# Performance work log

Measured on AMD Instinct MI355X. Metric: run time of the kernel, lower is better.

Reference implementation:

```python
import jax, jax.numpy as jnp
import numpy as np

N_NODES = 10000
N_EDGES = 160000
NEG_SLOPE = 0.2


def _gat_layer(x, src, dst, W, a_src, a_dst, bias, concat):
    # x: [N, F_in]; W: [F_in, H*C]; a_src/a_dst: [H, C]; bias: [H*C] or [C]
    N = x.shape[0]
    H, C = a_src.shape
    h = (x @ W).reshape(N, H, C)                       # [N,H,C]
    al_s = jnp.einsum('nhc,hc->nh', h, a_src)          # [N,H]
    al_d = jnp.einsum('nhc,hc->nh', h, a_dst)          # [N,H]
    e = jax.nn.leaky_relu(al_s[src] + al_d[dst], NEG_SLOPE)  # [E,H]
    # segment softmax over incoming edges of each destination node
    m = jax.ops.segment_max(e, dst, num_segments=N)    # [N,H]
    ex = jnp.exp(e - m[dst])
    denom = jax.ops.segment_sum(ex, dst, num_segments=N)
    alpha = ex / (denom[dst] + 1e-16)                  # [E,H]
    msg = h[src] * alpha[:, :, None]                   # [E,H,C]
    out = jax.ops.segment_sum(msg, dst, num_segments=N)  # [N,H,C]
    out = out.reshape(N, H * C) if concat else out.mean(axis=1)
    return out + bias


def setup_inputs() -> dict:
    key = jax.random.key(0)
    ks = jax.random.split(key, 10)
    in_dim, hid, out_dim, heads = 768, 512, 768, 4
    x = jax.random.normal(ks[0], (N_NODES, in_dim), dtype=jnp.float32)
    edge_index = jax.random.randint(ks[1], (2, N_EDGES), 0, N_NODES, dtype=jnp.int64)
    g = lambda k, shape, fan: jax.random.normal(k, shape, jnp.float32) / np.sqrt(fan)
    return {
        'x': x,
        'edge_index': edge_index,
        'W1': g(ks[2], (in_dim, heads * hid), in_dim),
        'att_src1': g(ks[3], (heads, hid), hid),
        'att_dst1': g(ks[4], (heads, hid), hid),
        'b1': jnp.zeros((heads * hid,), jnp.float32),
        'W2': g(ks[5], (heads * hid, out_dim), heads * hid),
        'att_src2': g(ks[6], (1, out_dim), out_dim),
        'att_dst2': g(ks[7], (1, out_dim), out_dim),
        'b2': jnp.zeros((out_dim,), jnp.float32),
    }


def reference(x, edge_index, W1, att_src1, att_dst1, b1, W2, att_src2, att_dst2, b2):
    N = x.shape[0]
    loops = jnp.arange(N, dtype=edge_index.dtype)
    src = jnp.concatenate([edge_index[0], loops])  # PyG GATConv adds self-loops
    dst = jnp.concatenate([edge_index[1], loops])
    h = jax.nn.elu(_gat_layer(x, src, dst, W1, att_src1, att_dst1, b1, concat=True))
    out = _gat_layer(h, src, dst, W2, att_src2, att_dst2, b2, concat=False)
    return out
```

## Files before the change

### kernel.cpp

```cpp
#include <hip/hip_runtime.h>
#include <hip/hip_bf16.h>
#include <math.h>

#define N_NODES 10000
#define N_EDGES0 160000
#define E_TOT (N_EDGES0 + N_NODES)
#define H1 4
#define C1 512
#define F1 2048
#define IN_DIM 768
#define C2 768
#define NEG_SLOPE 0.2f

typedef _Float16 f16x8 __attribute__((ext_vector_type(8)));
typedef _Float16 f16x4 __attribute__((ext_vector_type(4)));
typedef float f32x4 __attribute__((ext_vector_type(4)));

typedef __attribute__((address_space(1))) const void* gas_ptr;
typedef __attribute__((address_space(3))) void* las_ptr;
static __device__ __forceinline__ void gload16(const void* g, void* l) {
  __builtin_amdgcn_global_load_lds((gas_ptr)g, (las_ptr)l, 16, 0, 0);
}

static __device__ __forceinline__ unsigned enc_f(float v) {
  unsigned u = __float_as_uint(v);
  return (u & 0x80000000u) ? ~u : (u | 0x80000000u);
}
static __device__ __forceinline__ float dec_f(unsigned u) {
  return (u & 0x80000000u) ? __uint_as_float(u ^ 0x80000000u)
                           : __uint_as_float(~u);
}

static __device__ __forceinline__ void edge_sd(const int* __restrict__ ei, int e,
                                               int& s, int& d) {
  if (e < N_EDGES0) { s = ei[e]; d = ei[N_EDGES0 + e]; }
  else { s = e - N_EDGES0; d = s; }
}

__global__ void tsplit_k(const float* __restrict__ W, _Float16* __restrict__ hi,
                         _Float16* __restrict__ lo, int K, int N) {
  __shared__ float tile[32][33];
  const int nb = blockIdx.x * 32, kb = blockIdx.y * 32;
  const int tx = threadIdx.x, ty = threadIdx.y;
  for (int r = ty; r < 32; r += 8)
    tile[r][tx] = W[(size_t)(kb + r) * N + nb + tx];
  __syncthreads();
  for (int r = ty; r < 32; r += 8) {
    float v = tile[tx][r];
    _Float16 h = (_Float16)v;
    hi[(size_t)(nb + r) * K + kb + tx] = h;
    lo[(size_t)(nb + r) * K + kb + tx] = (_Float16)(v - (float)h);
  }
}

__global__ void proj_attn_k(const float* __restrict__ W1,
                            const float* __restrict__ as1,
                            const float* __restrict__ ad1,
                            float* __restrict__ ws, float* __restrict__ wd) {
  int wv = (blockIdx.x * blockDim.x + threadIdx.x) >> 6;
  int lane = threadIdx.x & 63;
  if (wv >= H1 * IN_DIM) return;
  int h = wv / IN_DIM, k = wv - h * IN_DIM;
  const float* wrow = W1 + (size_t)k * F1 + h * C1;
  const float* sa = as1 + h * C1;
  const float* da = ad1 + h * C1;
  float ss = 0.f, sd = 0.f;
  for (int c = lane; c < C1; c += 64) {
    float v = wrow[c];
    ss = fmaf(v, sa[c], ss);
    sd = fmaf(v, da[c], sd);
  }
#pragma unroll
  for (int o = 32; o; o >>= 1) { ss += __shfl_xor(ss, o); sd += __shfl_xor(sd, o); }
  if (lane == 0) { ws[(size_t)h * IN_DIM + k] = ss; wd[(size_t)h * IN_DIM + k] = sd; }
}

__global__ void logits1_k(const float* __restrict__ x,
                          const float* __restrict__ ws, const float* __restrict__ wd,
                          float* __restrict__ als, float* __restrict__ ald) {
  int n = (blockIdx.x * blockDim.x + threadIdx.x) >> 6;
  int lane = threadIdx.x & 63;
  if (n >= N_NODES) return;
  const float* xp = x + (size_t)n * IN_DIM;
  float ss[H1] = {0.f, 0.f, 0.f, 0.f}, sd[H1] = {0.f, 0.f, 0.f, 0.f};
  for (int k = lane; k < IN_DIM; k += 64) {
    float xv = xp[k];
#pragma unroll
    for (int h = 0; h < H1; h++) {
      ss[h] = fmaf(xv, ws[h * IN_DIM + k], ss[h]);
      sd[h] = fmaf(xv, wd[h * IN_DIM + k], sd[h]);
    }
  }
#pragma unroll
  for (int h = 0; h < H1; h++)
#pragma unroll
    for (int o = 32; o; o >>= 1) { ss[h] += __shfl_xor(ss[h], o); sd[h] += __shfl_xor(sd[h], o); }
  if (lane == 0) {
#pragma unroll
    for (int h = 0; h < H1; h++) {
      als[(size_t)n * H1 + h] = ss[h];
      ald[(size_t)n * H1 + h] = sd[h];
    }
  }
}

template <bool SPLITOUT>
__global__ __launch_bounds__(256) void gemm_sf16(
    const _Float16* __restrict__ Ahi, const _Float16* __restrict__ Alo,
    const _Float16* __restrict__ Bhi, const _Float16* __restrict__ Blo,
    int M, int N, int K, int lda, int nch, int nbx, int nwg,
    float* __restrict__ C, const float* __restrict__ bias,
    _Float16* __restrict__ ohi, _Float16* __restrict__ olo,
    const float* __restrict__ asrc, const float* __restrict__ adst,
    float* __restrict__ als, float* __restrict__ ald, int Hh, int Cdim) {
  __shared__ _Float16 sAh[128 * 64];
  __shared__ _Float16 sAl[128 * 64];
  __shared__ _Float16 sBh[128 * 64];
  __shared__ _Float16 sBl[128 * 64];

  const int orig = blockIdx.x;
  const int q = nwg >> 3, rr = nwg & 7;
  const int xcd = orig & 7, pos = orig >> 3;
  const int wgid = (xcd < rr ? xcd * (q + 1) : rr * (q + 1) + (xcd - rr) * q) + pos;
  const int bx = wgid % nbx, by = wgid / nbx;
  const int m0 = by * 128, n0 = bx * 128;

  const int t = threadIdx.x;
  const int w = t >> 6, lane = t & 63;
  const size_t hofs = (size_t)(n0 / nch) * K;

  const int gsrc = ((lane & 7) - (lane >> 3)) & 7;
  const int ru = w * 8 + (lane >> 3);
  size_t gA[4], gB[4];
#pragma unroll
  for (int i = 0; i < 4; i++) {
    const int ra = min(m0 + i * 32 + ru, M - 1);
    gA[i] = (size_t)ra * lda + hofs + gsrc * 8;
    gB[i] = (size_t)(n0 + i * 32 + ru) * K + gsrc * 8;
  }

  const int wr = w >> 1, wc = w & 1;
  const int lr = lane & 15, lg = lane >> 4;

  f32x4 acc[4][4];
#pragma unroll
  for (int i = 0; i < 4; i++)
#pragma unroll
    for (int j = 0; j < 4; j++) acc[i][j] = (f32x4)(0.f);

  for (int k0 = 0; k0 < K; k0 += 64) {
    __syncthreads();
#pragma unroll
    for (int i = 0; i < 4; i++) {
      const int lofs = w * 1024 + i * 4096;
      gload16(Ahi + gA[i] + k0, (char*)sAh + lofs);
      gload16(Alo + gA[i] + k0, (char*)sAl + lofs);
      gload16(Bhi + gB[i] + k0, (char*)sBh + lofs);
      gload16(Blo + gB[i] + k0, (char*)sBl + lofs);
    }
    __syncthreads();

#pragma unroll
    for (int kk = 0; kk < 2; kk++) {
      const int ga = ((kk * 4 + lg + (lr & 7)) & 7) * 8;
      f16x8 ah[4], al[4], bh[4], bl[4];
#pragma unroll
      for (int i = 0; i < 4; i++) {
        const int ao = (wr * 64 + i * 16 + lr) * 64 + ga;
        const int bo = (wc * 64 + i * 16 + lr) * 64 + ga;
        ah[i] = *(const f16x8*)&sAh[ao];
        al[i] = *(const f16x8*)&sAl[ao];
        bh[i] = *(const f16x8*)&sBh[bo];
        bl[i] = *(const f16x8*)&sBl[bo];
      }
#pragma unroll
      for (int i = 0; i < 4; i++)
#pragma unroll
        for (int j = 0; j < 4; j++) {
          acc[i][j] = __builtin_amdgcn_mfma_f32_16x16x32_f16(ah[i], bh[j], acc[i][j], 0, 0, 0);
          acc[i][j] = __builtin_amdgcn_mfma_f32_16x16x32_f16(ah[i], bl[j], acc[i][j], 0, 0, 0);
          acc[i][j] = __builtin_amdgcn_mfma_f32_16x16x32_f16(al[i], bh[j], acc[i][j], 0, 0, 0);
        }
    }
  }

  if constexpr (SPLITOUT) {
#pragma unroll
    for (int j = 0; j < 4; j++) {
      const int col = n0 + wc * 64 + j * 16 + lr;
      const float bv = bias[col];
#pragma unroll
      for (int i = 0; i < 4; i++) {
        const int rbase = m0 + wr * 64 + i * 16 + lg * 4;
#pragma unroll
        for (int r = 0; r < 4; r++) {
          const int row = rbase + r;
          if (row < M) {
            float o = acc[i][j][r] + bv;
            o = o > 0.f ? o : expm1f(o);
            _Float16 hv = (_Float16)o;
            ohi[(size_t)row * N + col] = hv;
            olo[(size_t)row * N + col] = (_Float16)(o - (float)hv);
          }
        }
      }
    }
  } else {
#pragma unroll
    for (int i = 0; i < 4; i++)
#pragma unroll
      for (int j = 0; j < 4; j++) {
        const int col = n0 + wc * 64 + j * 16 + lr;
        const int rbase = m0 + wr * 64 + i * 16 + lg * 4;
#pragma unroll
        for (int r = 0; r < 4; r++) {
          int row = rbase + r;
          if (row < M) C[(size_t)row * N + col] = acc[i][j][r];
        }
      }

    const int head = n0 / Cdim;
    const int cbase = n0 - head * Cdim + wc * 64 + lr;
    float asv[4], adv[4];
#pragma unroll
    for (int j = 0; j < 4; j++) {
      asv[j] = asrc[(size_t)head * Cdim + cbase + j * 16];
      adv[j] = adst[(size_t)head * Cdim + cbase + j * 16];
    }
#pragma unroll
    for (int i = 0; i < 4; i++) {
      const int rbase = m0 + wr * 64 + i * 16 + lg * 4;
#pragma unroll
      for (int r = 0; r < 4; r++) {
        float ss = 0.f, sd = 0.f;
#pragma unroll
        for (int j = 0; j < 4; j++) {
          float v = acc[i][j][r];
          ss = fmaf(v, asv[j], ss);
          sd = fmaf(v, adv[j], sd);
        }
#pragma unroll
        for (int o = 8; o; o >>= 1) {
          ss += __shfl_xor(ss, o);
          sd += __shfl_xor(sd, o);
        }
        if (lr == 0 && rbase + r < M) {
          atomicAdd(&als[(size_t)(rbase + r) * Hh + head], ss);
          atomicAdd(&ald[(size_t)(rbase + r) * Hh + head], sd);
        }
      }
    }
  }
}

__global__ void edge_max_k(const int* __restrict__ ei,
                           const float* __restrict__ als,
                           const float* __restrict__ ald,
                           float* __restrict__ ev, unsigned* __restrict__ menc,
                           int Hh) {
  int idx = blockIdx.x * blockDim.x + threadIdx.x;
  if (idx >= E_TOT * Hh) return;
  int e = idx / Hh, hh = idx - e * Hh;
  int s, d; edge_sd(ei, e, s, d);
  float x = als[s * Hh + hh] + ald[d * Hh + hh];
  float v = x > 0.f ? x : NEG_SLOPE * x;
  ev[idx] = v;
  atomicMax(&menc[d * Hh + hh], enc_f(v));
}

__global__ void edge_exp_k(const int* __restrict__ ei,
                           const unsigned* __restrict__ menc,
                           const float* __restrict__ ev,
                           const int* __restrict__ csr_pos,
                           float* __restrict__ evs, float* __restrict__ denom,
                           int Hh) {
  int idx = blockIdx.x * blockDim.x + threadIdx.x;
  if (idx >= E_TOT * Hh) return;
  int e = idx / Hh, hh = idx - e * Hh;
  int s, d; edge_sd(ei, e, s, d);
  float m = dec_f(menc[d * Hh + hh]);
  float ex = expf(ev[idx] - m);
  evs[(size_t)csr_pos[e] * Hh + hh] = ex;
  atomicAdd(&denom[d * Hh + hh], ex);
}

__global__ void hist_k(const int* __restrict__ ei, int* __restrict__ count) {
  int e = blockIdx.x * blockDim.x + threadIdx.x;
  if (e >= E_TOT) return;
  int s, d; edge_sd(ei, e, s, d);
  atomicAdd(&count[d], 1);
}

__global__ __launch_bounds__(1024) void scan_k(const int* __restrict__ count,
                                               int* __restrict__ rowstart,
                                               int N, int total) {
  __shared__ int sums[1024];
  __shared__ int carry_s;
  int t = threadIdx.x;
  if (t == 0) carry_s = 0;
  __syncthreads();
  for (int base = 0; base < N; base += 1024) {
    int i = base + t;
    int c = (i < N) ? count[i] : 0;
    sums[t] = c;
    __syncthreads();
    for (int off = 1; off < 1024; off <<= 1) {
      int v = (t >= off) ? sums[t - off] : 0;
      __syncthreads();
      sums[t] += v;
      __syncthreads();
    }
    int carry = carry_s;
    if (i < N) rowstart[i] = carry + sums[t] - c;
    __syncthreads();
    if (t == 1023) carry_s = carry + sums[1023];
    __syncthreads();
  }
  if (t == 0) rowstart[N] = total;
}

__global__ void scatter_k(const int* __restrict__ ei,
                          const int* __restrict__ rowstart,
                          int* __restrict__ cursor,
                          int* __restrict__ csr_src, int* __restrict__ csr_pos) {
  int e = blockIdx.x * blockDim.x + threadIdx.x;
  if (e >= E_TOT) return;
  int s, d; edge_sd(ei, e, s, d);
  int pos = rowstart[d] + atomicAdd(&cursor[d], 1);
  csr_src[pos] = s;
  csr_pos[e] = pos;
}

__global__ __launch_bounds__(192) void aggregate_x_k(
    const float* __restrict__ x, const float* __restrict__ evs,
    const float* __restrict__ denom, const int* __restrict__ rowstart,
    const int* __restrict__ csr_src,
    _Float16* __restrict__ ohi, _Float16* __restrict__ olo) {
  const int n = blockIdx.x;
  const int f0 = threadIdx.x * 4;
  float inv[H1];
#pragma unroll
  for (int h = 0; h < H1; h++) inv[h] = 1.f / (denom[n * H1 + h] + 1e-16f);
  float acc[H1][4];
#pragma unroll
  for (int h = 0; h < H1; h++)
#pragma unroll
    for (int q = 0; q < 4; q++) acc[h][q] = 0.f;

  const int j0 = rowstart[n], j1 = rowstart[n + 1];
  int j = j0;
  for (; j + 4 <= j1; j += 4) {
    int sidx[4];
    float4 wv[4], xv[4];
#pragma unroll
    for (int u = 0; u < 4; u++) sidx[u] = csr_src[j + u];
#pragma unroll
    for (int u = 0; u < 4; u++) wv[u] = *(const float4*)&evs[(size_t)(j + u) * H1];
#pragma unroll
    for (int u = 0; u < 4; u++)
      xv[u] = *(const float4*)(x + (size_t)sidx[u] * IN_DIM + f0);
#pragma unroll
    for (int u = 0; u < 4; u++) {
      const float* pw = (const float*)&wv[u];
#pragma unroll
      for (int h = 0; h < H1; h++) {
        acc[h][0] = fmaf(pw[h], xv[u].x, acc[h][0]);
        acc[h][1] = fmaf(pw[h], xv[u].y, acc[h][1]);
        acc[h][2] = fmaf(pw[h], xv[u].z, acc[h][2]);
        acc[h][3] = fmaf(pw[h], xv[u].w, acc[h][3]);
      }
    }
  }
  for (; j < j1; j++) {
    int s = csr_src[j];
    float4 wv = *(const float4*)&evs[(size_t)j * H1];
    float4 xv = *(const float4*)(x + (size_t)s * IN_DIM + f0);
    const float* pw = (const float*)&wv;
#pragma unroll
    for (int h = 0; h < H1; h++) {
      acc[h][0] = fmaf(pw[h], xv.x, acc[h][0]);
      acc[h][1] = fmaf(pw[h], xv.y, acc[h][1]);
      acc[h][2] = fmaf(pw[h], xv.z, acc[h][2]);
      acc[h][3] = fmaf(pw[h], xv.w, acc[h][3]);
    }
  }

#pragma unroll
  for (int h = 0; h < H1; h++) {
    f16x4 h4, l4;
#pragma unroll
    for (int q = 0; q < 4; q++) {
      float o = acc[h][q] * inv[h];
      _Float16 hv = (_Float16)o;
      h4[q] = hv;
      l4[q] = (_Float16)(o - (float)hv);
    }
    *(f16x4*)&ohi[(size_t)n * (H1 * IN_DIM) + h * IN_DIM + f0] = h4;
    *(f16x4*)&olo[(size_t)n * (H1 * IN_DIM) + h * IN_DIM + f0] = l4;
  }
}

template <int FT>
__global__ __launch_bounds__(256) void aggregate_k(
    const float* __restrict__ hsrc, const float* __restrict__ evs,
    const float* __restrict__ denom, const float* __restrict__ bias,
    const int* __restrict__ rowstart, const int* __restrict__ csr_src,
    float* __restrict__ out, int Hh, int C) {
  const int n = blockIdx.x;
  const int t = threadIdx.x;
  const int F = Hh * C;
  const int f0 = t * FT;
  const int hh = f0 / C;
  const float inv = 1.f / (denom[n * Hh + hh] + 1e-16f);
  float acc[FT];
#pragma unroll
  for (int i = 0; i < FT; i++) acc[i] = 0.f;
  const int j0 = rowstart[n], j1 = rowstart[n + 1];

  constexpr int UN = 8;
  int j = j0;
  for (; j + UN <= j1; j += UN) {
    int   sidx[UN];
    float wv[UN];
#pragma unroll
    for (int u = 0; u < UN; u++) sidx[u] = csr_src[j + u];
#pragma unroll
    for (int u = 0; u < UN; u++) wv[u] = evs[(size_t)(j + u) * Hh + hh];
    float4 va[UN][FT / 4];
#pragma unroll
    for (int u = 0; u < UN; u++) {
      const float* hp = hsrc + (size_t)sidx[u] * F + f0;
#pragma unroll
      for (int q = 0; q < FT / 4; q++) va[u][q] = *(const float4*)(hp + q * 4);
    }
#pragma unroll
    for (int u = 0; u < UN; u++)
#pragma unroll
      for (int q = 0; q < FT / 4; q++) {
        acc[q * 4 + 0] = fmaf(wv[u], va[u][q].x, acc[q * 4 + 0]);
        acc[q * 4 + 1] = fmaf(wv[u], va[u][q].y, acc[q * 4 + 1]);
        acc[q * 4 + 2] = fmaf(wv[u], va[u][q].z, acc[q * 4 + 2]);
        acc[q * 4 + 3] = fmaf(wv[u], va[u][q].w, acc[q * 4 + 3]);
      }
  }
  for (; j < j1; j++) {
    int s = csr_src[j];
    float wgt = evs[(size_t)j * Hh + hh];
    const float* hp = hsrc + (size_t)s * F + f0;
#pragma unroll
    for (int q = 0; q < FT / 4; q++) {
      float4 v = *(const float4*)(hp + q * 4);
      acc[q * 4 + 0] = fmaf(wgt, v.x, acc[q * 4 + 0]);
      acc[q * 4 + 1] = fmaf(wgt, v.y, acc[q * 4 + 1]);
      acc[q * 4 + 2] = fmaf(wgt, v.z, acc[q * 4 + 2]);
      acc[q * 4 + 3] = fmaf(wgt, v.w, acc[q * 4 + 3]);
    }
  }
#pragma unroll
  for (int i = 0; i < FT; i++)
    out[(size_t)n * F + f0 + i] = acc[i] * inv + bias[f0 + i];
}

extern "C" void kernel_launch(void* const* d_in, const int* in_sizes, int n_in,
                              void* d_out, int out_size, void* d_ws, size_t ws_size,
                              hipStream_t stream) {
  const float* x   = (const float*)d_in[0];
  const int*   ei  = (const int*)d_in[1];
  const float* W1  = (const float*)d_in[2];
  const float* as1 = (const float*)d_in[3];
  const float* ad1 = (const float*)d_in[4];
  const float* b1  = (const float*)d_in[5];
  const float* W2  = (const float*)d_in[6];
  const float* as2 = (const float*)d_in[7];
  const float* ad2 = (const float*)d_in[8];
  const float* b2  = (const float*)d_in[9];
  float* out = (float*)d_out;

  char* p = (char*)d_ws;
  auto alloc = [&](size_t bytes) {
    char* r = p;
    p += (bytes + 255) & ~(size_t)255;
    return r;
  };
  _Float16* xahi  = (_Float16*)alloc((size_t)N_NODES * H1 * IN_DIM * 2);
  _Float16* xalo  = (_Float16*)alloc((size_t)N_NODES * H1 * IN_DIM * 2);
  _Float16* W1hi  = (_Float16*)alloc((size_t)IN_DIM * F1 * 2);
  _Float16* W1lo  = (_Float16*)alloc((size_t)IN_DIM * F1 * 2);
  _Float16* W2hi  = (_Float16*)alloc((size_t)F1 * C2 * 2);
  _Float16* W2lo  = (_Float16*)alloc((size_t)F1 * C2 * 2);
  _Float16* h2hi  = (_Float16*)alloc((size_t)N_NODES * F1 * 2);
  _Float16* h2lo  = (_Float16*)alloc((size_t)N_NODES * F1 * 2);
  float*    ws1   = (float*)alloc((size_t)H1 * IN_DIM * 4);
  float*    wd1   = (float*)alloc((size_t)H1 * IN_DIM * 4);
  float*    als   = (float*)alloc((size_t)N_NODES * H1 * 4);
  float*    ald   = (float*)alloc((size_t)N_NODES * H1 * 4);
  unsigned* menc  = (unsigned*)alloc((size_t)N_NODES * H1 * 4);
  float*    denom = (float*)alloc((size_t)N_NODES * H1 * 4);
  float*    ev    = (float*)alloc((size_t)E_TOT * H1 * 4);
  float*    evs   = (float*)alloc((size_t)E_TOT * H1 * 4);
  int*      count    = (int*)alloc((size_t)N_NODES * 4);
  int*      rowstart = (int*)alloc((size_t)(N_NODES + 1) * 4);
  int*      cursor   = (int*)alloc((size_t)N_NODES * 4);
  int*      csr_src  = (int*)alloc((size_t)E_TOT * 4);
  int*      csr_pos  = (int*)alloc((size_t)E_TOT * 4);
  float*    h3 = (float*)xahi;

  const int EB = (E_TOT + 255) / 256;
  const int MT = (N_NODES + 127) / 128;

  hipMemsetAsync(count, 0, (size_t)N_NODES * 4, stream);
  hipMemsetAsync(cursor, 0, (size_t)N_NODES * 4, stream);
  hist_k<<<EB, 256, 0, stream>>>(ei, count);
  scan_k<<<1, 1024, 0, stream>>>(count, rowstart, N_NODES, E_TOT);
  scatter_k<<<EB, 256, 0, stream>>>(ei, rowstart, cursor, csr_src, csr_pos);

  tsplit_k<<<dim3(F1 / 32, IN_DIM / 32), dim3(32, 8), 0, stream>>>(W1, W1hi, W1lo,
                                                                   IN_DIM, F1);
  tsplit_k<<<dim3(C2 / 32, F1 / 32), dim3(32, 8), 0, stream>>>(W2, W2hi, W2lo,
                                                               F1, C2);
  proj_attn_k<<<(H1 * IN_DIM * 64) / 256, 256, 0, stream>>>(W1, as1, ad1, ws1, wd1);

  logits1_k<<<(N_NODES * 64 + 255) / 256, 256, 0, stream>>>(x, ws1, wd1, als, ald);
  hipMemsetAsync(menc, 0, (size_t)N_NODES * H1 * 4, stream);
  hipMemsetAsync(denom, 0, (size_t)N_NODES * H1 * 4, stream);
  edge_max_k<<<(E_TOT * H1 + 255) / 256, 256, 0, stream>>>(ei, als, ald, ev, menc, H1);
  edge_exp_k<<<(E_TOT * H1 + 255) / 256, 256, 0, stream>>>(ei, menc, ev, csr_pos,
                                                           evs, denom, H1);
  aggregate_x_k<<<N_NODES, 192, 0, stream>>>(x, evs, denom, rowstart, csr_src,
                                             xahi, xalo);
  {
    const int nbx = F1 / 128, nwg = nbx * MT;
    gemm_sf16<true><<<nwg, 256, 0, stream>>>(
        xahi, xalo, W1hi, W1lo, N_NODES, F1, IN_DIM, H1 * IN_DIM, C1, nbx, nwg,
        nullptr, b1, h2hi, h2lo, nullptr, nullptr, nullptr, nullptr, 0, C1);
  }

  hipMemsetAsync(als, 0, (size_t)N_NODES * 4, stream);
  hipMemsetAsync(ald, 0, (size_t)N_NODES * 4, stream);
  {
    const int nbx = C2 / 128, nwg = nbx * MT;
    gemm_sf16<false><<<nwg, 256, 0, stream>>>(
        h2hi, h2lo, W2hi, W2lo, N_NODES, C2, F1, F1, 1 << 30, nbx, nwg,
        h3, nullptr, nullptr, nullptr, as2, ad2, als, ald, 1, C2);
  }
  hipMemsetAsync(menc, 0, (size_t)N_NODES * 4, stream);
  hipMemsetAsync(denom, 0, (size_t)N_NODES * 4, stream);
  edge_max_k<<<EB, 256, 0, stream>>>(ei, als, ald, ev, menc, 1);
  edge_exp_k<<<EB, 256, 0, stream>>>(ei, menc, ev, csr_pos, evs, denom, 1);
  aggregate_k<4><<<N_NODES, 192, 0, stream>>>(h3, evs, denom, b2, rowstart,
                                              csr_src, out, 1, C2);
}
```

Before: 614.6 us.

## Double-buffer split-f16 GEMM LDS tiles with K-step of 32

Replaces the single-buffered 64-wide K tile with two 32-wide LDS buffers, so the next tile's global-to-LDS loads are issued before the MFMA work on the current tile and overlap with it. This removes one barrier per iteration and the exposed load latency. LDS footprint stays the same, but there are twice as many iterations and a new swizzle pattern, which adds barrier overhead and some risk of bank conflicts.

```diff
diff --git a/kernel.cpp b/kernel.cpp
--- a/kernel.cpp
+++ b/kernel.cpp
@@ -113,10 +113,7 @@
     _Float16* __restrict__ ohi, _Float16* __restrict__ olo,
     const float* __restrict__ asrc, const float* __restrict__ adst,
     float* __restrict__ als, float* __restrict__ ald, int Hh, int Cdim) {
-  __shared__ _Float16 sAh[128 * 64];
-  __shared__ _Float16 sAl[128 * 64];
-  __shared__ _Float16 sBh[128 * 64];
-  __shared__ _Float16 sBl[128 * 64];
+  __shared__ _Float16 sbuf[2][4][128 * 32];
 
   const int orig = blockIdx.x;
   const int q = nwg >> 3, rr = nwg & 7;
@@ -129,18 +126,21 @@
   const int w = t >> 6, lane = t & 63;
   const size_t hofs = (size_t)(n0 / nch) * K;
 
-  const int gsrc = ((lane & 7) - (lane >> 3)) & 7;
-  const int ru = w * 8 + (lane >> 3);
-  size_t gA[4], gB[4];
-#pragma unroll
-  for (int i = 0; i < 4; i++) {
-    const int ra = min(m0 + i * 32 + ru, M - 1);
-    gA[i] = (size_t)ra * lda + hofs + gsrc * 8;
-    gB[i] = (size_t)(n0 + i * 32 + ru) * K + gsrc * 8;
-  }
+  const int o0 = w * 1024 + lane * 16;
+  const int o1 = o0 + 4096;
+  const int ma0 = o0 >> 6, ma1 = o1 >> 6;
+  const int gsrc = ((lane & 3) - ((lane >> 3) & 3)) & 3;
+  const int rA0 = min(m0 + ma0, M - 1), rA1 = min(m0 + ma1, M - 1);
+  const size_t gA0 = (size_t)rA0 * lda + hofs + gsrc * 8;
+  const size_t gA1 = (size_t)rA1 * lda + hofs + gsrc * 8;
+  const size_t gB0 = (size_t)(n0 + ma0) * K + gsrc * 8;
+  const size_t gB1 = (size_t)(n0 + ma1) * K + gsrc * 8;
 
   const int wr = w >> 1, wc = w & 1;
   const int lr = lane & 15, lg = lane >> 4;
+  const int lgs = (lg + (lr >> 1)) & 3;
+  const int aoff = (wr * 64 + lr) * 32 + lgs * 8;
+  const int boff = (wc * 64 + lr) * 32 + lgs * 8;
 
   f32x4 acc[4][4];
 #pragma unroll
@@ -148,40 +148,52 @@
 #pragma unroll
     for (int j = 0; j < 4; j++) acc[i][j] = (f32x4)(0.f);
 
-  for (int k0 = 0; k0 < K; k0 += 64) {
+  auto STAGE = [&](int b, int k0) {
+    char* a0 = (char*)&sbuf[b][0][0] + w * 1024;
+    char* a1 = (char*)&sbuf[b][1][0] + w * 1024;
+    char* b0 = (char*)&sbuf[b][2][0] + w * 1024;
+    char* b1 = (char*)&sbuf[b][3][0] + w * 1024;
+    gload16(Ahi + gA0 + k0, a0);
+    gload16(Ahi + gA1 + k0, a0 + 4096);
+    gload16(Alo + gA0 + k0, a1);
+    gload16(Alo + gA1 + k0, a1 + 4096);
+    gload16(Bhi + gB0 + k0, b0);
+    gload16(Bhi + gB1 + k0, b0 + 4096);
+    gload16(Blo + gB0 + k0, b1);
+    gload16(Blo + gB1 + k0, b1 + 4096);
+  };
+
+  const int NT = K >> 5;
+  STAGE(0, 0);
+  __syncthreads();
+
+  int cur = 0;
+  for (int ts = 0; ts < NT; ++ts) {
+    if (ts + 1 < NT) STAGE(cur ^ 1, (ts + 1) * 32);
+
+    const _Float16* pAh = &sbuf[cur][0][0];
+    const _Float16* pAl = &sbuf[cur][1][0];
+    const _Float16* pBh = &sbuf[cur][2][0];
+    const _Float16* pBl = &sbuf[cur][3][0];
+    f16x8 ah[4], al[4], bh[4], bl[4];
+#pragma unroll
+    for (int i = 0; i < 4; i++) {
+      ah[i] = *(const f16x8*)&pAh[aoff + i * 16 * 32];
+      al[i] = *(const f16x8*)&pAl[aoff + i * 16 * 32];
+      bh[i] = *(const f16x8*)&pBh[boff + i * 16 * 32];
+      bl[i] = *(const f16x8*)&pBl[boff + i * 16 * 32];
+    }
+#pragma unroll
+    for (int i = 0; i < 4; i++)
+#pragma unroll
+      for (int j = 0; j < 4; j++) {
+        acc[i][j] = __builtin_amdgcn_mfma_f32_16x16x32_f16(ah[i], bh[j], acc[i][j], 0, 0, 0);
+        acc[i][j] = __builtin_amdgcn_mfma_f32_16x16x32_f16(ah[i], bl[j], acc[i][j], 0, 0, 0);
+        acc[i][j] = __builtin_amdgcn_mfma_f32_16x16x32_f16(al[i], bh[j], acc[i][j], 0, 0, 0);
+      }
+
     __syncthreads();
-#pragma unroll
-    for (int i = 0; i < 4; i++) {
-      const int lofs = w * 1024 + i * 4096;
-      gload16(Ahi + gA[i] + k0, (char*)sAh + lofs);
-      gload16(Alo + gA[i] + k0, (char*)sAl + lofs);
-      gload16(Bhi + gB[i] + k0, (char*)sBh + lofs);
-      gload16(Blo + gB[i] + k0, (char*)sBl + lofs);
-    }
-    __syncthreads();
-
-#pragma unroll
-    for (int kk = 0; kk < 2; kk++) {
-      const int ga = ((kk * 4 + lg + (lr & 7)) & 7) * 8;
-      f16x8 ah[4], al[4], bh[4], bl[4];
-#pragma unroll
-      for (int i = 0; i < 4; i++) {
-        const int ao = (wr * 64 + i * 16 + lr) * 64 + ga;
-        const int bo = (wc * 64 + i * 16 + lr) * 64 + ga;
-        ah[i] = *(const f16x8*)&sAh[ao];
-        al[i] = *(const f16x8*)&sAl[ao];
-        bh[i] = *(const f16x8*)&sBh[bo];
-        bl[i] = *(const f16x8*)&sBl[bo];
-      }
-#pragma unroll
-      for (int i = 0; i < 4; i++)
-#pragma unroll
-        for (int j = 0; j < 4; j++) {
-          acc[i][j] = __builtin_amdgcn_mfma_f32_16x16x32_f16(ah[i], bh[j], acc[i][j], 0, 0, 0);
-          acc[i][j] = __builtin_amdgcn_mfma_f32_16x16x32_f16(ah[i], bl[j], acc[i][j], 0, 0, 0);
-          acc[i][j] = __builtin_amdgcn_mfma_f32_16x16x32_f16(al[i], bh[j], acc[i][j], 0, 0, 0);
-        }
-    }
+    cur ^= 1;
   }
 
   if constexpr (SPLITOUT) {
```

New measurement: 619.7 us. No clear change (+0.8%).
